# Optimization experiments

Measured on AMD Instinct MI355X. Metric: run time of the kernel, lower is better.

Reference implementation:

```python
import jax, jax.numpy as jnp
import numpy as np

SCALE = 1.0 / np.sqrt(7.0)  # window_size ** 0.5 with window_size=7


def setup_inputs() -> dict:
    key = jax.random.key(0)
    ks = jax.random.split(key, 7)
    B, C, H, W = 8, 64, 64, 64
    O = 64
    x = jax.random.normal(ks[0], (B, C, H, W), dtype=jnp.float32)
    s = 1.0 / np.sqrt(C)
    Wq = jax.random.normal(ks[1], (O, C), dtype=jnp.float32) * s
    bq = jax.random.normal(ks[2], (O,), dtype=jnp.float32) * 0.01
    Wk = jax.random.normal(ks[3], (O, C), dtype=jnp.float32) * s
    bk = jax.random.normal(ks[4], (O,), dtype=jnp.float32) * 0.01
    Wv = jax.random.normal(ks[5], (O, C), dtype=jnp.float32) * s
    bv = jax.random.normal(ks[6], (O,), dtype=jnp.float32) * 0.01
    return {"x": x, "Wq": Wq, "bq": bq, "Wk": Wk, "bk": bk, "Wv": Wv, "bv": bv}


def reference(x, Wq, bq, Wk, bk, Wv, bv):
    B, C, H, W = x.shape
    O = Wq.shape[0]
    N = H * W
    # 1x1 convs == per-pixel linear projections
    xf = x.reshape(B, C, N)  # [B, C, N]
    q = jnp.einsum('bcn,oc->bon', xf, Wq) + bq[None, :, None]  # [B, O, N]
    k = jnp.einsum('bcn,oc->bon', xf, Wk) + bk[None, :, None]
    v = jnp.einsum('bcn,oc->bon', xf, Wv) + bv[None, :, None]
    # global attention over all H*W positions
    attn = jnp.einsum('bcn,bcm->bnm', q, k) * SCALE  # [B, N, N]
    attn = jax.nn.softmax(attn, axis=-1)
    out = jnp.einsum('bnm,bcm->bnc', attn, v)  # [B, N, O]
    # faithful to torch's out.view(B, -1, H, W): raw row-major reshape of [B, N, O]
    return out.reshape(B, O, H, W)
```

## Files before the change

kernel.cpp:

```cpp
#include <hip/hip_runtime.h>
#include <math.h>

#define B_ 8
#define N_ 4096
#define SCALE2_ 0.54528747f

typedef __bf16 bf16x8 __attribute__((ext_vector_type(8)));
typedef float f32x4 __attribute__((ext_vector_type(4)));
typedef float f32x16 __attribute__((ext_vector_type(16)));
typedef unsigned short ushortx8 __attribute__((ext_vector_type(8)));
typedef unsigned short ushort;
typedef unsigned int uint;
typedef uint uint2v __attribute__((ext_vector_type(2)));

static __device__ __forceinline__ ushort f2bf(float f) {
  union { float f; unsigned u; } v; v.f = f;
  unsigned r = v.u + 0x7FFFu + ((v.u >> 16) & 1u);
  return (ushort)(r >> 16);
}
static __device__ __forceinline__ uint pk2(float a, float b) {
  union { __bf16 h[2]; uint u; } v;
  v.h[0] = (__bf16)a; v.h[1] = (__bf16)b;
  return v.u;
}

__global__ __launch_bounds__(256)
void proj_kernel(const float* __restrict__ x,
                 const float* __restrict__ Wq, const float* __restrict__ bq,
                 const float* __restrict__ Wk, const float* __restrict__ bk,
                 const float* __restrict__ Wv, const float* __restrict__ bv,
                 ushort* __restrict__ Qb, ushort* __restrict__ Kb,
                 ushort* __restrict__ Vt)
{
  __shared__ ushort sm[256][17];

  const int tid = threadIdx.x;
  const int gp  = (blockIdx.x << 8) + tid;
  const int b   = gp >> 12;
  const int y   = blockIdx.y;
  const int mat = y >> 2;
  const int o0  = (y & 3) << 4;
  const int n   = gp & 4095;

  const float* xb = x + ((size_t)b << 18) + n;
  float xr[64];
  #pragma unroll
  for (int c = 0; c < 64; ++c) xr[c] = xb[(size_t)c << 12];

  const float* W    = (mat == 0) ? Wq : (mat == 1) ? Wk : Wv;
  const float* bias = (mat == 0) ? bq : (mat == 1) ? bk : bv;

  float acc[16];
  #pragma unroll 1
  for (int j = 0; j < 16; ++j) {
    const float4* wr = (const float4*)(W + ((o0 + j) << 6));
    float a = bias[o0 + j];
    #pragma unroll
    for (int c4 = 0; c4 < 16; ++c4) {
      float4 w4 = wr[c4];
      a += w4.x * xr[4*c4] + w4.y * xr[4*c4+1] + w4.z * xr[4*c4+2] + w4.w * xr[4*c4+3];
    }
    acc[j] = a;
  }

  if (mat == 2) {
    #pragma unroll
    for (int j = 0; j < 16; ++j) sm[tid][j] = f2bf(acc[j]);
    __syncthreads();
    const int ol = tid >> 4;
    const int p0 = (tid & 15) << 4;
    uint pk[8];
    #pragma unroll
    for (int i = 0; i < 16; ++i) {
      ushort v = sm[p0 + i][ol];
      if (i & 1) pk[i >> 1] |= (uint)v << 16; else pk[i >> 1] = v;
    }
    const int nb = (blockIdx.x << 8) & 4095;
    ushort* dst = Vt + ((((size_t)b << 6) + o0 + ol) << 12) + nb + p0;
    *(ushortx8*)dst       = *(ushortx8*)&pk[0];
    *(ushortx8*)(dst + 8) = *(ushortx8*)&pk[4];
  } else {
    const float scl = (mat == 0) ? SCALE2_ : 1.0f;
    ushort* D = (mat == 0) ? Qb : Kb;
    __align__(16) ushort hv[16];
    #pragma unroll
    for (int j = 0; j < 16; ++j) hv[j] = f2bf(acc[j] * scl);
    const size_t base = ((size_t)gp << 6) + o0;
    *(ushortx8*)(D + base)     = *(const ushortx8*)&hv[0];
    *(ushortx8*)(D + base + 8) = *(const ushortx8*)&hv[8];
  }
}

__global__ __launch_bounds__(256, 4)
void flash_kernel(const ushort* __restrict__ Qb, const ushort* __restrict__ Kb,
                  const ushort* __restrict__ Vt, float* __restrict__ out)
{
  __shared__ __align__(16) ushort KL[2][64][72];
  __shared__ __align__(16) ushort VL[2][64][72];

  const int tid  = threadIdx.x;
  const int lane = tid & 63;
  const int w    = tid >> 6;
  const int qg   = w >> 1;
  const int kh   = w & 1;
  const int r32  = lane & 31;
  const int h    = lane >> 5;
  const int h8   = h << 3;

  const int bidx = (blockIdx.x & 7) * 64 + (blockIdx.x >> 3);
  const int b  = bidx >> 6;
  const int qw = ((bidx & 63) << 6) + (qg << 5);

  const ushort* KbB = Kb + ((size_t)b << 18);
  const ushort* VtB = Vt + ((size_t)b << 18);

  bf16x8 qf[4];
  {
    const ushort* qp = Qb + ((((size_t)b << 12) + qw + r32) << 6) + h8;
    #pragma unroll
    for (int ks = 0; ks < 4; ++ks) qf[ks] = *(const bf16x8*)(qp + (ks << 4));
  }

  const int srow = tid >> 3;
  const int scg  = (tid & 7) << 3;

  ushortx8 rk0, rk1, rv0, rv1;
  #define STAGE_LOAD(c0) do { \
    rk0 = *(const ushortx8*)(KbB + (((size_t)((c0) + srow)) << 6) + scg); \
    rk1 = *(const ushortx8*)(KbB + (((size_t)((c0) + srow + 32)) << 6) + scg); \
    rv0 = *(const ushortx8*)(VtB + ((size_t)srow << 12) + (c0) + scg); \
    rv1 = *(const ushortx8*)(VtB + ((size_t)(srow + 32) << 12) + (c0) + scg); \
  } while (0)
  #define STAGE_WRITE(bf) do { \
    *(ushortx8*)&KL[bf][srow][scg]      = rk0; \
    *(ushortx8*)&KL[bf][srow + 32][scg] = rk1; \
    *(ushortx8*)&VL[bf][srow][scg]      = rv0; \
    *(ushortx8*)&VL[bf][srow + 32][scg] = rv1; \
  } while (0)

  STAGE_LOAD(0);
  STAGE_WRITE(0);

  const f32x16 Z = (f32x16)(0.0f);
  f32x16 acc0 = Z, acc1 = Z;
  float l_lane = 0.f;
  int cur = 0;

  const int krow = (kh << 5) + r32;
  const int vcb  = (kh << 5) + h8;

  for (int t = 0; t < 64; ++t) {
    __syncthreads();
    if (t < 63) STAGE_LOAD((t + 1) << 6);

    bf16x8 kf0 = *(const bf16x8*)&KL[cur][krow][h8];
    f32x16 s = __builtin_amdgcn_mfma_f32_32x32x16_bf16(kf0, qf[0], Z, 0, 0, 0);
    #pragma unroll
    for (int ks = 1; ks < 4; ++ks) {
      bf16x8 kf = *(const bf16x8*)&KL[cur][krow][(ks << 4) + h8];
      s = __builtin_amdgcn_mfma_f32_32x32x16_bf16(kf, qf[ks], s, 0, 0, 0);
    }

    float rs = 0.f;
    #pragma unroll
    for (int i = 0; i < 16; ++i) {
      float p = __builtin_exp2f(s[i]);
      s[i] = p;
      rs += p;
    }
    l_lane += rs;

    bf16x8 pb[2];
    #pragma unroll
    for (int c = 0; c < 2; ++c) {
      const int base = c << 3;
      uint plo0 = pk2(s[base+0], s[base+1]);
      uint plo1 = pk2(s[base+2], s[base+3]);
      uint phi0 = pk2(s[base+4], s[base+5]);
      uint phi1 = pk2(s[base+6], s[base+7]);
      uint2v r0 = __builtin_amdgcn_permlane32_swap(plo0, phi0, false, false);
      uint2v r1 = __builtin_amdgcn_permlane32_swap(plo1, phi1, false, false);
      union { uint u[4]; bf16x8 v; } f_;
      f_.u[0] = r0.x;
      f_.u[1] = r1.x;
      f_.u[2] = r0.y;
      f_.u[3] = r1.y;
      pb[c] = f_.v;
    }

    #pragma unroll
    for (int ks = 0; ks < 2; ++ks) {
      const int co = vcb + (ks << 4);
      bf16x8 v0 = *(const bf16x8*)&VL[cur][r32][co];
      acc0 = __builtin_amdgcn_mfma_f32_32x32x16_bf16(v0, pb[ks], acc0, 0, 0, 0);
      bf16x8 v1 = *(const bf16x8*)&VL[cur][32 + r32][co];
      acc1 = __builtin_amdgcn_mfma_f32_32x32x16_bf16(v1, pb[ks], acc1, 0, 0, 0);
    }

    if (t < 63) STAGE_WRITE(cur ^ 1);
    cur ^= 1;
  }

  float l_me = l_lane + __shfl_xor(l_lane, 32);

  __syncthreads();
  float* cmb = (float*)KL;
  if (kh == 1) {
    float* p = cmb + ((qg << 6) + lane) * 33;
    #pragma unroll
    for (int i = 0; i < 16; ++i) { p[i] = acc0[i]; p[16 + i] = acc1[i]; }
    p[32] = l_me;
  }
  __syncthreads();
  if (kh == 0) {
    const float* p = cmb + ((qg << 6) + lane) * 33;
    const float inv = 1.0f / (l_me + p[32]);
    const size_t rowb = (((size_t)b << 12) + qw + r32) << 6;
    #pragma unroll
    for (int g = 0; g < 4; ++g) {
      f32x4 o4;
      #pragma unroll
      for (int i = 0; i < 4; ++i)
        o4[i] = (acc0[4*g + i] + p[4*g + i]) * inv;
      *(f32x4*)(out + rowb + (g << 3) + (h << 2)) = o4;
    }
    #pragma unroll
    for (int g = 0; g < 4; ++g) {
      f32x4 o4;
      #pragma unroll
      for (int i = 0; i < 4; ++i)
        o4[i] = (acc1[4*g + i] + p[16 + 4*g + i]) * inv;
      *(f32x4*)(out + rowb + 32 + (g << 3) + (h << 2)) = o4;
    }
  }
  #undef STAGE_LOAD
  #undef STAGE_WRITE
}

extern "C" void kernel_launch(void* const* d_in, const int* in_sizes, int n_in,
                              void* d_out, int out_size, void* d_ws, size_t ws_size,
                              hipStream_t stream) {
  (void)in_sizes; (void)n_in; (void)out_size; (void)ws_size;
  const float* x  = (const float*)d_in[0];
  const float* Wq = (const float*)d_in[1];
  const float* bq = (const float*)d_in[2];
  const float* Wk = (const float*)d_in[3];
  const float* bk = (const float*)d_in[4];
  const float* Wv = (const float*)d_in[5];
  const float* bv = (const float*)d_in[6];
  float* out = (float*)d_out;

  const size_t SZ = (size_t)B_ * N_ * 64;
  ushort* Qb = (ushort*)d_ws;
  ushort* Kb = Qb + SZ;
  ushort* Vt = Kb + SZ;

  proj_kernel<<<dim3(128, 12), dim3(256), 0, stream>>>(x, Wq, bq, Wk, bk, Wv, bv,
                                                       Qb, Kb, Vt);
  flash_kernel<<<dim3(B_ * (N_ / 64)), dim3(256), 0, stream>>>(Qb, Kb, Vt, out);
}
```

Before: 87.89 us.

## Split KV range across two blocks per query tile and add combine kernel

Each query tile's key/value range is split into two halves handled by separate blocks, doubling the grid to fill more CU slots. The first half writes unnormalized output to out, the second writes to a workspace buffer, and both write row sums. A new combine kernel adds the partials and normalizes. This raises parallelism at the cost of extra global memory traffic and an additional kernel launch.

Result: slower. 93.33 us (+6.2%).

```diff
diff --git a/kernel.cpp b/kernel.cpp
--- a/kernel.cpp
+++ b/kernel.cpp
@@ -93,7 +93,8 @@
 
 __global__ __launch_bounds__(256, 4)
 void flash_kernel(const ushort* __restrict__ Qb, const ushort* __restrict__ Kb,
-                  const ushort* __restrict__ Vt, float* __restrict__ out)
+                  const ushort* __restrict__ Vt, float* __restrict__ out,
+                  float* __restrict__ Opart, float* __restrict__ Lp)
 {
   __shared__ __align__(16) ushort KL[2][64][72];
   __shared__ __align__(16) ushort VL[2][64][72];
@@ -107,9 +108,13 @@
   const int h    = lane >> 5;
   const int h8   = h << 3;
 
-  const int bidx = (blockIdx.x & 7) * 64 + (blockIdx.x >> 3);
-  const int b  = bidx >> 6;
-  const int qw = ((bidx & 63) << 6) + (qg << 5);
+  const int bidx = (blockIdx.x & 7) * 128 + (blockIdx.x >> 3);
+  const int b   = bidx >> 7;
+  const int rem = bidx & 127;
+  const int qt  = rem >> 1;
+  const int sp  = rem & 1;
+  const int qw  = (qt << 6) + (qg << 5);
+  const int kvb = sp << 11;
 
   const ushort* KbB = Kb + ((size_t)b << 18);
   const ushort* VtB = Vt + ((size_t)b << 18);
@@ -138,7 +143,7 @@
     *(ushortx8*)&VL[bf][srow + 32][scg] = rv1; \
   } while (0)
 
-  STAGE_LOAD(0);
+  STAGE_LOAD(kvb);
   STAGE_WRITE(0);
 
   const f32x16 Z = (f32x16)(0.0f);
@@ -149,9 +154,9 @@
   const int krow = (kh << 5) + r32;
   const int vcb  = (kh << 5) + h8;
 
-  for (int t = 0; t < 64; ++t) {
+  for (int t = 0; t < 32; ++t) {
     __syncthreads();
-    if (t < 63) STAGE_LOAD((t + 1) << 6);
+    if (t < 31) STAGE_LOAD(kvb + ((t + 1) << 6));
 
     bf16x8 kf0 = *(const bf16x8*)&KL[cur][krow][h8];
     f32x16 s = __builtin_amdgcn_mfma_f32_32x32x16_bf16(kf0, qf[0], Z, 0, 0, 0);
@@ -197,7 +202,7 @@
       acc1 = __builtin_amdgcn_mfma_f32_32x32x16_bf16(v1, pb[ks], acc1, 0, 0, 0);
     }
 
-    if (t < 63) STAGE_WRITE(cur ^ 1);
+    if (t < 31) STAGE_WRITE(cur ^ 1);
     cur ^= 1;
   }
 
@@ -214,27 +219,43 @@
   __syncthreads();
   if (kh == 0) {
     const float* p = cmb + ((qg << 6) + lane) * 33;
-    const float inv = 1.0f / (l_me + p[32]);
+    const float ltot = l_me + p[32];
+    float* dst = sp ? Opart : out;
     const size_t rowb = (((size_t)b << 12) + qw + r32) << 6;
+    if (h == 0) Lp[(sp << 15) + (b << 12) + qw + r32] = ltot;
     #pragma unroll
     for (int g = 0; g < 4; ++g) {
       f32x4 o4;
       #pragma unroll
       for (int i = 0; i < 4; ++i)
-        o4[i] = (acc0[4*g + i] + p[4*g + i]) * inv;
-      *(f32x4*)(out + rowb + (g << 3) + (h << 2)) = o4;
+        o4[i] = acc0[4*g + i] + p[4*g + i];
+      *(f32x4*)(dst + rowb + (g << 3) + (h << 2)) = o4;
     }
     #pragma unroll
     for (int g = 0; g < 4; ++g) {
       f32x4 o4;
       #pragma unroll
       for (int i = 0; i < 4; ++i)
-        o4[i] = (acc1[4*g + i] + p[16 + 4*g + i]) * inv;
-      *(f32x4*)(out + rowb + 32 + (g << 3) + (h << 2)) = o4;
+        o4[i] = acc1[4*g + i] + p[16 + 4*g + i];
+      *(f32x4*)(dst + rowb + 32 + (g << 3) + (h << 2)) = o4;
     }
   }
   #undef STAGE_LOAD
   #undef STAGE_WRITE
+}
+
+__global__ __launch_bounds__(256)
+void combine_kernel(float* __restrict__ out, const float* __restrict__ Opart,
+                    const float* __restrict__ Lp)
+{
+  const int e   = ((blockIdx.x << 8) + threadIdx.x) << 2;
+  const int row = e >> 6;
+  const float inv = 1.0f / (Lp[row] + Lp[32768 + row]);
+  f32x4 a = *(f32x4*)(out + e);
+  f32x4 bb = *(const f32x4*)(Opart + e);
+  #pragma unroll
+  for (int i = 0; i < 4; ++i) a[i] = (a[i] + bb[i]) * inv;
+  *(f32x4*)(out + e) = a;
 }
 
 extern "C" void kernel_launch(void* const* d_in, const int* in_sizes, int n_in,
@@ -254,8 +275,11 @@
   ushort* Qb = (ushort*)d_ws;
   ushort* Kb = Qb + SZ;
   ushort* Vt = Kb + SZ;
+  float*  Op = (float*)(Vt + SZ);
+  float*  Lp = Op + SZ;
 
   proj_kernel<<<dim3(128, 12), dim3(256), 0, stream>>>(x, Wq, bq, Wk, bk, Wv, bv,
                                                        Qb, Kb, Vt);
-  flash_kernel<<<dim3(B_ * (N_ / 64)), dim3(256), 0, stream>>>(Qb, Kb, Vt, out);
-}
+  flash_kernel<<<dim3(1024), dim3(256), 0, stream>>>(Qb, Kb, Vt, out, Op, Lp);
+  combine_kernel<<<dim3(2048), dim3(256), 0, stream>>>(out, Op, Lp);
+}
```
